# Kernel tuning notes

Measured on AMD Instinct MI355X. Metric: run time of the kernel, lower is better.

## Reference

```python
import jax, jax.numpy as jnp
import numpy as np

B, T, D_IN, H, S, DH = 128, 256, 512, 1024, 128, 1024

def _lin(key, out_d, in_d):
    k = 1.0 / np.sqrt(in_d)
    return jax.random.uniform(key, (out_d, in_d), jnp.float32, -k, k)

def setup_inputs() -> dict:
    key = jax.random.key(0)
    ks = jax.random.split(key, 16)
    kH = 1.0 / np.sqrt(H)
    return {
        'x': jax.random.normal(ks[0], (B, T, D_IN), jnp.float32),
        'noise': jax.random.normal(ks[1], (B, T, S), jnp.float32),
        # LSTM (torch gate order: i, f, g, o)
        'W_ih': _lin(ks[2], 4 * H, S),
        'W_hh': _lin(ks[3], 4 * H, H),
        'b_ih': jax.random.uniform(ks[4], (4 * H,), jnp.float32, -kH, kH),
        'b_hh': jax.random.uniform(ks[5], (4 * H,), jnp.float32, -kH, kH),
        # posterior heads over concat(x_t, h_t): in = H + D_IN
        'Wm': _lin(ks[6], S, H + D_IN), 'bm': jnp.zeros((S,), jnp.float32),
        'Wv': _lin(ks[7], S, H + D_IN), 'bv': jnp.zeros((S,), jnp.float32),
        # decoder MLP
        'Wd1': _lin(ks[8], DH, S), 'bd1': jnp.zeros((DH,), jnp.float32),
        'Wd2': _lin(ks[9], D_IN, DH), 'bd2': jnp.zeros((D_IN,), jnp.float32),
    }

def reference(x, noise, W_ih, W_hh, b_ih, b_hh, Wm, bm, Wv, bv, Wd1, bd1, Wd2, bd2):
    Bb = x.shape[0]
    Hh = W_hh.shape[1]
    Ss = Wm.shape[0]
    dt = x.dtype

    def step(carry, inp):
        h, c, z = carry          # [B,H], [B,H], [B,S]
        xt, nt = inp             # [B,D_IN], [B,S]
        gates = z @ W_ih.T + b_ih + h @ W_hh.T + b_hh   # [B,4H]
        i, f, g, o = jnp.split(gates, 4, axis=-1)
        c = jax.nn.sigmoid(f) * c + jax.nn.sigmoid(i) * jnp.tanh(g)
        h = jax.nn.sigmoid(o) * jnp.tanh(c)
        pi = jnp.concatenate([xt, h], axis=-1)           # [B, D_IN+H]
        mean = pi @ Wm.T + bm
        log_var = pi @ Wv.T + bv
        std = jnp.exp(0.5 * log_var)
        z_new = nt * std + mean
        kl = jnp.sum(std * std + mean * mean - jnp.log(std) - 0.5)
        return (h, c, z_new), (z_new, kl)

    init = (jnp.zeros((Bb, Hh), dt), jnp.zeros((Bb, Hh), dt), jnp.zeros((Bb, Ss), dt))
    xs = (jnp.swapaxes(x, 0, 1), jnp.swapaxes(noise, 0, 1))  # time-major
    _, (zs, kls) = jax.lax.scan(step, init, xs)
    z = jnp.swapaxes(zs, 0, 1)                                # [B,T,S]
    kl = jnp.sum(kls)
    x_hat = jax.nn.relu(z @ Wd1.T + bd1) @ Wd2.T + bd2        # [B,T,D_IN]
    return x_hat, kl
```

## Files before the change

### kernel.cpp

```cpp
#include <hip/hip_runtime.h>
#include <hip/hip_bf16.h>

#define Bdim 128
#define Tdim 256
#define DIN 512
#define Hdim 1024
#define Sdim 128
#define DHdim 1024
#define KG 1152
#define KP 1536
#define NBLK 192
#define LDP 1160

using short8  = __attribute__((ext_vector_type(8))) short;
using floatx4 = __attribute__((ext_vector_type(4))) float;
typedef unsigned long long ull;

#define MFMA(a, b, c) __builtin_amdgcn_mfma_f32_16x16x32_bf16((a), (b), (c), 0, 0, 0)

#define XBF_OFF   0ull
#define WG_OFF    33554432ull
#define WMV_OFF   42991616ull
#define HB_OFF    0ull
#define WD1_OFF   67108864ull
#define WD2_OFF   67371008ull
#define AB_OFF    68419584ull
#define AB_SZ     294912ull
#define ZALL_OFF  69009408ull
#define KL_OFF    77398016ull
#define FLG_OFF   77398144ull

__device__ __forceinline__ float sigf(float v) { return 1.0f / (1.0f + __expf(-v)); }
__device__ __forceinline__ float tanhfast(float v) { return 1.0f - 2.0f / (__expf(2.0f * v) + 1.0f); }

__device__ __forceinline__ short8 cload16(const __hip_bfloat16* p) {
  short8 r;
  asm volatile("global_load_dwordx4 %0, %1, off sc0 sc1" : "=&v"(r) : "v"(p));
  return r;
}
#define VMWAIT0()                                              \
  do {                                                         \
    asm volatile("s_waitcnt vmcnt(0)" ::: "memory");           \
    __builtin_amdgcn_sched_barrier(0);                         \
  } while (0)
#define SB0() __builtin_amdgcn_sched_barrier(0)

__device__ __forceinline__ void astore8(__hip_bfloat16* p, ull v) {
  __hip_atomic_store((ull*)(void*)p, v, __ATOMIC_RELAXED, __HIP_MEMORY_SCOPE_AGENT);
}

__device__ __forceinline__ void waitflags(unsigned* flags, int base, int mask,
                                          unsigned target, int lane) {
  unsigned* p = flags + base + (lane & mask);
  while (!__all((int)(__hip_atomic_load(p, __ATOMIC_RELAXED, __HIP_MEMORY_SCOPE_AGENT) >= target))) {
    __builtin_amdgcn_s_sleep(8);
  }
}

__global__ __launch_bounds__(256) void prep_kernel(
    const float* __restrict__ x, const float* __restrict__ W_ih,
    const float* __restrict__ W_hh, const float* __restrict__ Wm,
    const float* __restrict__ Wv, const float* __restrict__ Wd1,
    const float* __restrict__ Wd2, char* __restrict__ ws) {
  long long i = (long long)blockIdx.x * 256 + threadIdx.x;
  if (i < 16777216LL) {
    ((__hip_bfloat16*)(ws + XBF_OFF))[i] = __float2bfloat16(x[i]);
    return;
  }
  i -= 16777216LL;
  if (i < 4718592LL) {
    int j = (int)(i / KG), k = (int)(i % KG);
    float v = (k < Sdim) ? W_ih[j * Sdim + k] : W_hh[(long long)j * Hdim + (k - Sdim)];
    ((__hip_bfloat16*)(ws + WG_OFF))[i] = __float2bfloat16(v);
    return;
  }
  i -= 4718592LL;
  if (i < 393216LL) {
    int r = (int)(i / KP), k = (int)(i % KP);
    float v = (r < Sdim) ? Wm[r * KP + k] : Wv[(r - Sdim) * KP + k];
    ((__hip_bfloat16*)(ws + WMV_OFF))[i] = __float2bfloat16(v);
    return;
  }
  i -= 393216LL;
  if (i < 131072LL) { ((__hip_bfloat16*)(ws + WD1_OFF))[i] = __float2bfloat16(Wd1[i]); return; }
  i -= 131072LL;
  if (i < 524288LL) { ((__hip_bfloat16*)(ws + WD2_OFF))[i] = __float2bfloat16(Wd2[i]); return; }
  i -= 524288LL;
  if (i < 147456LL) { ((__hip_bfloat16*)(ws + AB_OFF))[i] = __float2bfloat16(0.0f); return; }
  i -= 147456LL;
  if (i == 0) { *((float*)(ws + KL_OFF)) = 0.0f; return; }
  i -= 1;
  if (i < 192LL) { ((unsigned*)(ws + FLG_OFF))[i] = 0u; return; }
}

__global__ __launch_bounds__(256, 1) void scan_kernel(
    char* __restrict__ ws, const float* __restrict__ noise,
    const float* __restrict__ b_ih, const float* __restrict__ b_hh,
    const float* __restrict__ bm, const float* __restrict__ bv) {
  const __hip_bfloat16* WG = (const __hip_bfloat16*)(ws + WG_OFF);
  const __hip_bfloat16* WMV = (const __hip_bfloat16*)(ws + WMV_OFF);
  const __hip_bfloat16* xbf = (const __hip_bfloat16*)(ws + XBF_OFF);
  __hip_bfloat16* zall = (__hip_bfloat16*)(ws + ZALL_OFF);
  float* klacc = (float*)(ws + KL_OFF);
  unsigned* flags = (unsigned*)(ws + FLG_OFF);

  __shared__ __align__(16) char ldsraw[16 * LDP * 2];
  __hip_bfloat16* lds = (__hip_bfloat16*)ldsraw;
  float* smem = (float*)ldsraw;

  const int tid = threadIdx.x;
  const int lane = tid & 63;
  const int w = tid >> 6;
  const int row16 = lane & 15;
  const int quad = lane >> 4;
  const int bid = blockIdx.x;
  const bool is_gates = (bid < 128);

  const __hip_bfloat16* gb_bp[4];
  float biasv[4];
  int mgrp = 0, ns = 0, rowbase = 0;
  float creg[4] = {0.f, 0.f, 0.f, 0.f};
  const __hip_bfloat16* hd_bpm = nullptr;
  const __hip_bfloat16* hd_bpv = nullptr;
  int hd_mb = 0, hd_sb = 0, hd_nx = 0, hd_kbase = 0;
  float hbm = 0.f, hbv = 0.f;
  float klw = 0.f;

  if (is_gates) {
    mgrp = bid >> 4;
    ns = bid & 15;
    rowbase = mgrp * 16;
    #pragma unroll
    for (int j = 0; j < 4; j++) {
      int idx = j * Hdim + ns * 64 + w * 16 + row16;
      gb_bp[j] = WG + (size_t)idx * KG;
      biasv[j] = b_ih[idx] + b_hh[idx];
    }
  } else {
    int hb = bid - 128;
    hd_mb = hb >> 3;
    hd_sb = hb & 7;
    int s = hd_sb * 16 + row16;
    hd_bpm = WMV + (size_t)s * KP;
    hd_bpv = WMV + (size_t)(128 + s) * KP;
    hbm = bm[s];
    hbv = bv[s];
    hd_kbase = w * 384;
    hd_nx = (hd_kbase < DIN) ? ((DIN - hd_kbase) >> 5) : 0;
    if (hd_nx > 12) hd_nx = 12;
  }

  for (int t = 0; t < Tdim; t++) {
    const int par = t & 1;
    const __hip_bfloat16* Ab = (const __hip_bfloat16*)(ws + AB_OFF + (ull)par * AB_SZ);
    __hip_bfloat16* AbW = (__hip_bfloat16*)(ws + AB_OFF + (ull)(par ^ 1) * AB_SZ);

    if (is_gates) {
      floatx4 acc[4];
      #pragma unroll
      for (int j = 0; j < 4; j++)
        acc[j] = (floatx4){biasv[j], biasv[j], biasv[j], biasv[j]};

      if (w == 0) waitflags(flags, mgrp * 16, 15, (unsigned)t, lane);
      __syncthreads();
      {
        short8 sreg[8];
        #pragma unroll
        for (int i = 0; i < 8; i++) {
          int s = tid + i * 256;
          sreg[i] = cload16(Ab + (size_t)(rowbase + (s >> 7)) * KG + Sdim + (s & 127) * 8);
        }
        VMWAIT0();
        #pragma unroll
        for (int i = 0; i < 8; i++) {
          int s = tid + i * 256;
          *(short8*)&lds[(s >> 7) * LDP + Sdim + (s & 127) * 8] = sreg[i];
        }
      }
      __syncthreads();
      #pragma unroll
      for (int c = 0; c < 8; c++) {
        #pragma unroll
        for (int i = 0; i < 4; i++) {
          const int k0 = Sdim + (c * 4 + i) * 32 + quad * 8;
          short8 a = *(const short8*)&lds[row16 * LDP + k0];
          #pragma unroll
          for (int j = 0; j < 4; j++)
            acc[j] = MFMA(a, *(const short8*)(gb_bp[j] + k0), acc[j]);
        }
        SB0();
      }
      if (w == 0) waitflags(flags, 128 + mgrp * 8, 7, (unsigned)t, lane);
      __syncthreads();
      {
        short8 zs = cload16(Ab + (size_t)(rowbase + (tid >> 4)) * KG + (tid & 15) * 8);
        VMWAIT0();
        *(short8*)&lds[(tid >> 4) * LDP + (tid & 15) * 8] = zs;
      }
      __syncthreads();
      #pragma unroll
      for (int kt = 0; kt < 4; kt++) {
        const int k0 = kt * 32 + quad * 8;
        short8 a = *(const short8*)&lds[row16 * LDP + k0];
        #pragma unroll
        for (int j = 0; j < 4; j++)
          acc[j] = MFMA(a, *(const short8*)(gb_bp[j] + k0), acc[j]);
      }
      SB0();
      int hc = ns * 64 + w * 16 + row16;
      #pragma unroll
      for (int r = 0; r < 4; r++) {
        float cn = sigf(acc[1][r]) * creg[r] + sigf(acc[0][r]) * tanhfast(acc[2][r]);
        creg[r] = cn;
        float hn = sigf(acc[3][r]) * tanhfast(cn);
        __hip_bfloat16 hbf = __float2bfloat16(hn);
        unsigned hu = (unsigned)reinterpret_cast<unsigned short&>(hbf);
        unsigned up = hu | (__shfl_xor(hu, 1, 64) << 16);
        unsigned uq = __shfl_xor(up, 2, 64);
        if ((row16 & 3) == 0) {
          int grow = rowbase + quad * 4 + r;
          astore8(AbW + (size_t)grow * KG + Sdim + hc, (ull)up | ((ull)uq << 32));
        }
      }
      __syncthreads();
      if (tid == 0)
        __hip_atomic_store(&flags[bid], (unsigned)(t + 1),
                           __ATOMIC_RELAXED, __HIP_MEMORY_SCOPE_AGENT);
    } else {
      float nz[4];
      if (w == 0) {
        #pragma unroll
        for (int r = 0; r < 4; r++) {
          int b = hd_mb * 16 + quad * 4 + r;
          int s = hd_sb * 16 + row16;
          nz[r] = noise[((size_t)b * Tdim + t) * Sdim + s];
        }
      }
      const __hip_bfloat16* axp = xbf + ((size_t)(hd_mb * 16 + row16) * Tdim + t) * DIN;
      const __hip_bfloat16* ahp = AbW + (size_t)(hd_mb * 16 + row16) * KG + Sdim;
      floatx4 am, av;
      if (w == 0) { am = (floatx4){hbm, hbm, hbm, hbm}; av = (floatx4){hbv, hbv, hbv, hbv}; }
      else        { am = (floatx4){0.f, 0.f, 0.f, 0.f}; av = (floatx4){0.f, 0.f, 0.f, 0.f}; }
      #pragma unroll
      for (int kt = 0; kt < 12; kt++) {
        if (kt < hd_nx) {
          int k0 = hd_kbase + kt * 32 + quad * 8;
          short8 a = *(const short8*)(axp + k0);
          am = MFMA(a, *(const short8*)(hd_bpm + k0), am);
          av = MFMA(a, *(const short8*)(hd_bpv + k0), av);
        }
      }
      if (w == 0) waitflags(flags, hd_mb * 16, 15, (unsigned)(t + 1), lane);
      __syncthreads();
      short8 hreg[12];
      #pragma unroll
      for (int kt = 0; kt < 12; kt++) {
        if (kt >= hd_nx)
          hreg[kt] = cload16(ahp + hd_kbase + kt * 32 + quad * 8 - DIN);
      }
      VMWAIT0();
      #pragma unroll
      for (int kt = 0; kt < 12; kt++) {
        if (kt >= hd_nx) {
          int k0 = hd_kbase + kt * 32 + quad * 8;
          am = MFMA(hreg[kt], *(const short8*)(hd_bpm + k0), am);
          av = MFMA(hreg[kt], *(const short8*)(hd_bpv + k0), av);
        }
      }
      SB0();
      #pragma unroll
      for (int r = 0; r < 4; r++) {
        smem[(w * 2 + 0) * 256 + lane * 4 + r] = am[r];
        smem[(w * 2 + 1) * 256 + lane * 4 + r] = av[r];
      }
      __syncthreads();
      if (w == 0) {
        #pragma unroll
        for (int r = 0; r < 4; r++) {
          int idx = lane * 4 + r;
          float mean = smem[0 * 256 + idx] + smem[2 * 256 + idx] +
                       smem[4 * 256 + idx] + smem[6 * 256 + idx];
          float lv = smem[1 * 256 + idx] + smem[3 * 256 + idx] +
                     smem[5 * 256 + idx] + smem[7 * 256 + idx];
          int b = hd_mb * 16 + quad * 4 + r;
          int s = hd_sb * 16 + row16;
          float std = __expf(0.5f * lv);
          float z = nz[r] * std + mean;
          __hip_bfloat16 zb = __float2bfloat16(z);
          zall[((size_t)b * Tdim + t) * Sdim + s] = zb;
          unsigned zu = (unsigned)reinterpret_cast<unsigned short&>(zb);
          unsigned up = zu | (__shfl_xor(zu, 1, 64) << 16);
          unsigned uq = __shfl_xor(up, 2, 64);
          if ((row16 & 3) == 0)
            astore8(AbW + (size_t)b * KG + s, (ull)up | ((ull)uq << 32));
          klw += std * std + mean * mean - 0.5f * lv - 0.5f;
        }
      }
      __syncthreads();
      if (tid == 0)
        __hip_atomic_store(&flags[bid], (unsigned)(t + 1),
                           __ATOMIC_RELAXED, __HIP_MEMORY_SCOPE_AGENT);
    }
  }
  if (!is_gates && w == 0) {
    #pragma unroll
    for (int off = 32; off > 0; off >>= 1) klw += __shfl_down(klw, off, 64);
    if (lane == 0) atomicAdd(klacc, klw);
  }
}

__global__ __launch_bounds__(256) void dec1_kernel(char* __restrict__ ws,
                                                   const float* __restrict__ bd1) {
  const __hip_bfloat16* zall = (const __hip_bfloat16*)(ws + ZALL_OFF);
  const __hip_bfloat16* Wd1b = (const __hip_bfloat16*)(ws + WD1_OFF);
  __hip_bfloat16* Hbuf = (__hip_bfloat16*)(ws + HB_OFF);
  int tid = threadIdx.x, lane = tid & 63, w = tid >> 6;
  int mb = blockIdx.x, nb = blockIdx.y;
  int row16 = lane & 15, quad = lane >> 4;
  int arow = mb * 64 + w * 16 + row16;
  const __hip_bfloat16* aptr = zall + (size_t)arow * Sdim;
  floatx4 acc[4] = {{0.f,0.f,0.f,0.f},{0.f,0.f,0.f,0.f},{0.f,0.f,0.f,0.f},{0.f,0.f,0.f,0.f}};
  #pragma unroll
  for (int kt = 0; kt < Sdim / 32; kt++) {
    int k0 = kt * 32 + quad * 8;
    short8 a = *(const short8*)(aptr + k0);
    #pragma unroll
    for (int j = 0; j < 4; j++) {
      const __hip_bfloat16* bp = Wd1b + (size_t)(nb * 64 + j * 16 + row16) * Sdim;
      acc[j] = MFMA(a, *(const short8*)(bp + k0), acc[j]);
    }
  }
  #pragma unroll
  for (int j = 0; j < 4; j++) {
    int n = nb * 64 + j * 16 + row16;
    float bias = bd1[n];
    #pragma unroll
    for (int r = 0; r < 4; r++) {
      int rr = mb * 64 + w * 16 + quad * 4 + r;
      float v = fmaxf(acc[j][r] + bias, 0.0f);
      Hbuf[(size_t)rr * DHdim + n] = __float2bfloat16(v);
    }
  }
}

__global__ __launch_bounds__(256) void dec2_kernel(char* __restrict__ ws,
                                                   const float* __restrict__ bd2,
                                                   float* __restrict__ out) {
  const __hip_bfloat16* Hbuf = (const __hip_bfloat16*)(ws + HB_OFF);
  const __hip_bfloat16* Wd2b = (const __hip_bfloat16*)(ws + WD2_OFF);
  int tid = threadIdx.x, lane = tid & 63, w = tid >> 6;
  int mb = blockIdx.x, nb = blockIdx.y;
  int row16 = lane & 15, quad = lane >> 4;
  int arow = mb * 64 + w * 16 + row16;
  const __hip_bfloat16* aptr = Hbuf + (size_t)arow * DHdim;
  const __hip_bfloat16* bp[4];
  #pragma unroll
  for (int j = 0; j < 4; j++) bp[j] = Wd2b + (size_t)(nb * 64 + j * 16 + row16) * DHdim;
  floatx4 acc[4] = {{0.f,0.f,0.f,0.f},{0.f,0.f,0.f,0.f},{0.f,0.f,0.f,0.f},{0.f,0.f,0.f,0.f}};
  for (int kt = 0; kt < DHdim / 32; kt++) {
    int k0 = kt * 32 + quad * 8;
    short8 a = *(const short8*)(aptr + k0);
    #pragma unroll
    for (int j = 0; j < 4; j++)
      acc[j] = MFMA(a, *(const short8*)(bp[j] + k0), acc[j]);
  }
  #pragma unroll
  for (int j = 0; j < 4; j++) {
    int n = nb * 64 + j * 16 + row16;
    float bias = bd2[n];
    #pragma unroll
    for (int r = 0; r < 4; r++) {
      int rr = mb * 64 + w * 16 + quad * 4 + r;
      out[(size_t)rr * DIN + n] = acc[j][r] + bias;
    }
  }
}

__global__ void kl_write_kernel(const char* __restrict__ ws, float* __restrict__ out) {
  if (threadIdx.x == 0 && blockIdx.x == 0)
    out[16777216] = *(const float*)(ws + KL_OFF);
}

extern "C" void kernel_launch(void* const* d_in, const int* in_sizes, int n_in,
                              void* d_out, int out_size, void* d_ws, size_t ws_size,
                              hipStream_t stream) {
  const float* x = (const float*)d_in[0];
  const float* noise = (const float*)d_in[1];
  const float* W_ih = (const float*)d_in[2];
  const float* W_hh = (const float*)d_in[3];
  const float* b_ih = (const float*)d_in[4];
  const float* b_hh = (const float*)d_in[5];
  const float* Wm = (const float*)d_in[6];
  const float* bm = (const float*)d_in[7];
  const float* Wv = (const float*)d_in[8];
  const float* bv = (const float*)d_in[9];
  const float* Wd1 = (const float*)d_in[10];
  const float* bd1 = (const float*)d_in[11];
  const float* Wd2 = (const float*)d_in[12];
  const float* bd2 = (const float*)d_in[13];
  char* ws = (char*)d_ws;
  float* out = (float*)d_out;

  long long total_prep = 22692033LL;
  int pblocks = (int)((total_prep + 255) / 256);
  prep_kernel<<<pblocks, 256, 0, stream>>>(x, W_ih, W_hh, Wm, Wv, Wd1, Wd2, ws);
  scan_kernel<<<NBLK, 256, 0, stream>>>(ws, noise, b_ih, b_hh, bm, bv);
  dec1_kernel<<<dim3(512, 16), 256, 0, stream>>>(ws, bd1);
  dec2_kernel<<<dim3(512, 8), 256, 0, stream>>>(ws, bd2, out);
  kl_write_kernel<<<1, 64, 0, stream>>>(ws, out);
}
```

Before: 5.527 ms.

## Split scan gate K-loop across 8 waves and consolidate head blocks

The persistent scan kernel now runs 512 threads per block. In the gate blocks, two wave halves each take half of the recurrent K dimension, and the partial sums are reduced through LDS before the LSTM cell update. Head blocks drop from 64 to 32; each block handles two S-tiles and stages h into LDS once instead of every wave loading it from global memory. The flag-polling sleep is also shortened. Together these aim to cut per-timestep latency on the serial critical path, at the cost of an extra LDS reduction and more synchronisation per step.

```diff
diff --git a/kernel.cpp b/kernel.cpp
--- a/kernel.cpp
+++ b/kernel.cpp
@@ -9,8 +9,11 @@
 #define DHdim 1024
 #define KG 1152
 #define KP 1536
-#define NBLK 192
+#define GBLK 128
+#define HBLK 32
+#define NBLK 160
 #define LDP 1160
+#define HP  1032
 
 using short8  = __attribute__((ext_vector_type(8))) short;
 using floatx4 = __attribute__((ext_vector_type(4))) float;
@@ -53,7 +56,7 @@
                                           unsigned target, int lane) {
   unsigned* p = flags + base + (lane & mask);
   while (!__all((int)(__hip_atomic_load(p, __ATOMIC_RELAXED, __HIP_MEMORY_SCOPE_AGENT) >= target))) {
-    __builtin_amdgcn_s_sleep(8);
+    __builtin_amdgcn_s_sleep(4);
   }
 }
 
@@ -93,7 +96,7 @@
   if (i < 192LL) { ((unsigned*)(ws + FLG_OFF))[i] = 0u; return; }
 }
 
-__global__ __launch_bounds__(256, 1) void scan_kernel(
+__global__ __launch_bounds__(512, 1) void scan_kernel(
     char* __restrict__ ws, const float* __restrict__ noise,
     const float* __restrict__ b_ih, const float* __restrict__ b_hh,
     const float* __restrict__ bm, const float* __restrict__ bv) {
@@ -104,9 +107,8 @@
   float* klacc = (float*)(ws + KL_OFF);
   unsigned* flags = (unsigned*)(ws + FLG_OFF);
 
-  __shared__ __align__(16) char ldsraw[16 * LDP * 2];
+  __shared__ __align__(16) char ldsraw[57600];
   __hip_bfloat16* lds = (__hip_bfloat16*)ldsraw;
-  float* smem = (float*)ldsraw;
 
   const int tid = threadIdx.x;
   const int lane = tid & 63;
@@ -114,15 +116,15 @@
   const int row16 = lane & 15;
   const int quad = lane >> 4;
   const int bid = blockIdx.x;
-  const bool is_gates = (bid < 128);
+  const bool is_gates = (bid < GBLK);
 
   const __hip_bfloat16* gb_bp[4];
   float biasv[4];
-  int mgrp = 0, ns = 0, rowbase = 0;
+  int mgrp = 0, ns = 0, rowbase = 0, cs = 0, khalf = 0;
   float creg[4] = {0.f, 0.f, 0.f, 0.f};
   const __hip_bfloat16* hd_bpm = nullptr;
   const __hip_bfloat16* hd_bpv = nullptr;
-  int hd_mb = 0, hd_sb = 0, hd_nx = 0, hd_kbase = 0;
+  int hd_mb = 0, hd_pg = 0, hd_nx = 0, hd_kbase = 0, hd_g = 0, hd_stile = 0;
   float hbm = 0.f, hbv = 0.f;
   float klw = 0.f;
 
@@ -130,22 +132,27 @@
     mgrp = bid >> 4;
     ns = bid & 15;
     rowbase = mgrp * 16;
+    cs = w & 3;
+    khalf = w >> 2;
     #pragma unroll
     for (int j = 0; j < 4; j++) {
-      int idx = j * Hdim + ns * 64 + w * 16 + row16;
+      int idx = j * Hdim + ns * 64 + cs * 16 + row16;
       gb_bp[j] = WG + (size_t)idx * KG;
       biasv[j] = b_ih[idx] + b_hh[idx];
     }
   } else {
-    int hb = bid - 128;
-    hd_mb = hb >> 3;
-    hd_sb = hb & 7;
-    int s = hd_sb * 16 + row16;
+    int hb = bid - GBLK;
+    hd_mb = hb >> 2;
+    hd_pg = hb & 3;
+    hd_g = w >> 2;
+    hd_stile = hd_pg * 2 + hd_g;
+    int s = hd_stile * 16 + row16;
     hd_bpm = WMV + (size_t)s * KP;
     hd_bpv = WMV + (size_t)(128 + s) * KP;
     hbm = bm[s];
     hbv = bv[s];
-    hd_kbase = w * 384;
+    int kp = w & 3;
+    hd_kbase = kp * 384;
     hd_nx = (hd_kbase < DIN) ? ((DIN - hd_kbase) >> 5) : 0;
     if (hd_nx > 12) hd_nx = 12;
   }
@@ -156,33 +163,36 @@
     __hip_bfloat16* AbW = (__hip_bfloat16*)(ws + AB_OFF + (ull)(par ^ 1) * AB_SZ);
 
     if (is_gates) {
+      float* rsm = (float*)(ldsraw + 37120);
       floatx4 acc[4];
       #pragma unroll
       for (int j = 0; j < 4; j++)
-        acc[j] = (floatx4){biasv[j], biasv[j], biasv[j], biasv[j]};
+        acc[j] = (khalf == 0)
+          ? (floatx4){biasv[j], biasv[j], biasv[j], biasv[j]}
+          : (floatx4){0.f, 0.f, 0.f, 0.f};
 
       if (w == 0) waitflags(flags, mgrp * 16, 15, (unsigned)t, lane);
       __syncthreads();
       {
-        short8 sreg[8];
-        #pragma unroll
-        for (int i = 0; i < 8; i++) {
-          int s = tid + i * 256;
+        short8 sreg[4];
+        #pragma unroll
+        for (int i = 0; i < 4; i++) {
+          int s = tid + i * 512;
           sreg[i] = cload16(Ab + (size_t)(rowbase + (s >> 7)) * KG + Sdim + (s & 127) * 8);
         }
         VMWAIT0();
         #pragma unroll
-        for (int i = 0; i < 8; i++) {
-          int s = tid + i * 256;
+        for (int i = 0; i < 4; i++) {
+          int s = tid + i * 512;
           *(short8*)&lds[(s >> 7) * LDP + Sdim + (s & 127) * 8] = sreg[i];
         }
       }
       __syncthreads();
       #pragma unroll
-      for (int c = 0; c < 8; c++) {
+      for (int c = 0; c < 4; c++) {
         #pragma unroll
         for (int i = 0; i < 4; i++) {
-          const int k0 = Sdim + (c * 4 + i) * 32 + quad * 8;
+          const int k0 = Sdim + (khalf * 16 + c * 4 + i) * 32 + quad * 8;
           short8 a = *(const short8*)&lds[row16 * LDP + k0];
           #pragma unroll
           for (int j = 0; j < 4; j++)
@@ -190,36 +200,45 @@
         }
         SB0();
       }
-      if (w == 0) waitflags(flags, 128 + mgrp * 8, 7, (unsigned)t, lane);
-      __syncthreads();
-      {
-        short8 zs = cload16(Ab + (size_t)(rowbase + (tid >> 4)) * KG + (tid & 15) * 8);
+      if (khalf == 1) {
+        #pragma unroll
+        for (int j = 0; j < 4; j++)
+          *(floatx4*)&rsm[cs * 1280 + lane * 20 + j * 4] = acc[j];
+      }
+      if (w == 0) waitflags(flags, GBLK + mgrp * 4, 3, (unsigned)t, lane);
+      __syncthreads();
+      if (khalf == 0) {
+        const __hip_bfloat16* zp = Ab + (size_t)(rowbase + row16) * KG;
+        short8 zreg[4];
+        #pragma unroll
+        for (int kt = 0; kt < 4; kt++)
+          zreg[kt] = cload16(zp + kt * 32 + quad * 8);
         VMWAIT0();
-        *(short8*)&lds[(tid >> 4) * LDP + (tid & 15) * 8] = zs;
-      }
-      __syncthreads();
-      #pragma unroll
-      for (int kt = 0; kt < 4; kt++) {
-        const int k0 = kt * 32 + quad * 8;
-        short8 a = *(const short8*)&lds[row16 * LDP + k0];
+        #pragma unroll
+        for (int kt = 0; kt < 4; kt++) {
+          const int k0 = kt * 32 + quad * 8;
+          #pragma unroll
+          for (int j = 0; j < 4; j++)
+            acc[j] = MFMA(zreg[kt], *(const short8*)(gb_bp[j] + k0), acc[j]);
+        }
+        SB0();
         #pragma unroll
         for (int j = 0; j < 4; j++)
-          acc[j] = MFMA(a, *(const short8*)(gb_bp[j] + k0), acc[j]);
-      }
-      SB0();
-      int hc = ns * 64 + w * 16 + row16;
-      #pragma unroll
-      for (int r = 0; r < 4; r++) {
-        float cn = sigf(acc[1][r]) * creg[r] + sigf(acc[0][r]) * tanhfast(acc[2][r]);
-        creg[r] = cn;
-        float hn = sigf(acc[3][r]) * tanhfast(cn);
-        __hip_bfloat16 hbf = __float2bfloat16(hn);
-        unsigned hu = (unsigned)reinterpret_cast<unsigned short&>(hbf);
-        unsigned up = hu | (__shfl_xor(hu, 1, 64) << 16);
-        unsigned uq = __shfl_xor(up, 2, 64);
-        if ((row16 & 3) == 0) {
-          int grow = rowbase + quad * 4 + r;
-          astore8(AbW + (size_t)grow * KG + Sdim + hc, (ull)up | ((ull)uq << 32));
+          acc[j] += *(const floatx4*)&rsm[cs * 1280 + lane * 20 + j * 4];
+        #pragma unroll
+        for (int r = 0; r < 4; r++) {
+          float cn = sigf(acc[1][r]) * creg[r] + sigf(acc[0][r]) * tanhfast(acc[2][r]);
+          creg[r] = cn;
+          float hn = sigf(acc[3][r]) * tanhfast(cn);
+          __hip_bfloat16 hbf = __float2bfloat16(hn);
+          unsigned hu = (unsigned)reinterpret_cast<unsigned short&>(hbf);
+          unsigned up = hu | (__shfl_xor(hu, 1, 64) << 16);
+          unsigned uq = __shfl_xor(up, 2, 64);
+          if ((row16 & 3) == 0) {
+            int grow = rowbase + quad * 4 + r;
+            int hc = ns * 64 + cs * 16 + row16;
+            astore8(AbW + (size_t)grow * KG + Sdim + hc, (ull)up | ((ull)uq << 32));
+          }
         }
       }
       __syncthreads();
@@ -227,63 +246,79 @@
         __hip_atomic_store(&flags[bid], (unsigned)(t + 1),
                            __ATOMIC_RELAXED, __HIP_MEMORY_SCOPE_AGENT);
     } else {
+      float* smf = (float*)(ldsraw + 33024);
       float nz[4];
-      if (w == 0) {
+      if ((w & 3) == 0) {
         #pragma unroll
         for (int r = 0; r < 4; r++) {
           int b = hd_mb * 16 + quad * 4 + r;
-          int s = hd_sb * 16 + row16;
+          int s = hd_stile * 16 + row16;
           nz[r] = noise[((size_t)b * Tdim + t) * Sdim + s];
         }
       }
       const __hip_bfloat16* axp = xbf + ((size_t)(hd_mb * 16 + row16) * Tdim + t) * DIN;
-      const __hip_bfloat16* ahp = AbW + (size_t)(hd_mb * 16 + row16) * KG + Sdim;
-      floatx4 am, av;
-      if (w == 0) { am = (floatx4){hbm, hbm, hbm, hbm}; av = (floatx4){hbv, hbv, hbv, hbv}; }
-      else        { am = (floatx4){0.f, 0.f, 0.f, 0.f}; av = (floatx4){0.f, 0.f, 0.f, 0.f}; }
-      #pragma unroll
-      for (int kt = 0; kt < 12; kt++) {
-        if (kt < hd_nx) {
-          int k0 = hd_kbase + kt * 32 + quad * 8;
-          short8 a = *(const short8*)(axp + k0);
-          am = MFMA(a, *(const short8*)(hd_bpm + k0), am);
-          av = MFMA(a, *(const short8*)(hd_bpv + k0), av);
+      floatx4 am = {0.f, 0.f, 0.f, 0.f}, av = {0.f, 0.f, 0.f, 0.f};
+      {
+        short8 areg[12];
+        #pragma unroll
+        for (int kt = 0; kt < 12; kt++)
+          if (kt < hd_nx)
+            areg[kt] = *(const short8*)(axp + hd_kbase + kt * 32 + quad * 8);
+        #pragma unroll
+        for (int kt = 0; kt < 12; kt++) {
+          if (kt < hd_nx) {
+            int k0 = hd_kbase + kt * 32 + quad * 8;
+            am = MFMA(areg[kt], *(const short8*)(hd_bpm + k0), am);
+            av = MFMA(areg[kt], *(const short8*)(hd_bpv + k0), av);
+          }
         }
       }
       if (w == 0) waitflags(flags, hd_mb * 16, 15, (unsigned)(t + 1), lane);
       __syncthreads();
-      short8 hreg[12];
-      #pragma unroll
-      for (int kt = 0; kt < 12; kt++) {
-        if (kt >= hd_nx)
-          hreg[kt] = cload16(ahp + hd_kbase + kt * 32 + quad * 8 - DIN);
-      }
-      VMWAIT0();
+      {
+        short8 sreg[4];
+        #pragma unroll
+        for (int i = 0; i < 4; i++) {
+          int s = tid + i * 512;
+          sreg[i] = cload16(AbW + (size_t)(hd_mb * 16 + (s >> 7)) * KG + Sdim + (s & 127) * 8);
+        }
+        VMWAIT0();
+        #pragma unroll
+        for (int i = 0; i < 4; i++) {
+          int s = tid + i * 512;
+          *(short8*)&lds[(s >> 7) * HP + (s & 127) * 8] = sreg[i];
+        }
+      }
+      __syncthreads();
       #pragma unroll
       for (int kt = 0; kt < 12; kt++) {
         if (kt >= hd_nx) {
           int k0 = hd_kbase + kt * 32 + quad * 8;
-          am = MFMA(hreg[kt], *(const short8*)(hd_bpm + k0), am);
-          av = MFMA(hreg[kt], *(const short8*)(hd_bpv + k0), av);
+          short8 a = *(const short8*)&lds[row16 * HP + (k0 - DIN)];
+          am = MFMA(a, *(const short8*)(hd_bpm + k0), am);
+          av = MFMA(a, *(const short8*)(hd_bpv + k0), av);
         }
       }
       SB0();
-      #pragma unroll
-      for (int r = 0; r < 4; r++) {
-        smem[(w * 2 + 0) * 256 + lane * 4 + r] = am[r];
-        smem[(w * 2 + 1) * 256 + lane * 4 + r] = av[r];
-      }
-      __syncthreads();
-      if (w == 0) {
+      {
+        int kp = w & 3;
+        #pragma unroll
+        for (int r = 0; r < 4; r++) {
+          smf[hd_g * 2048 + (kp * 2 + 0) * 256 + lane * 4 + r] = am[r];
+          smf[hd_g * 2048 + (kp * 2 + 1) * 256 + lane * 4 + r] = av[r];
+        }
+      }
+      __syncthreads();
+      if ((w & 3) == 0) {
         #pragma unroll
         for (int r = 0; r < 4; r++) {
           int idx = lane * 4 + r;
-          float mean = smem[0 * 256 + idx] + smem[2 * 256 + idx] +
-                       smem[4 * 256 + idx] + smem[6 * 256 + idx];
-          float lv = smem[1 * 256 + idx] + smem[3 * 256 + idx] +
-                     smem[5 * 256 + idx] + smem[7 * 256 + idx];
+          float mean = hbm + smf[hd_g * 2048 + 0 * 256 + idx] + smf[hd_g * 2048 + 2 * 256 + idx] +
+                       smf[hd_g * 2048 + 4 * 256 + idx] + smf[hd_g * 2048 + 6 * 256 + idx];
+          float lv = hbv + smf[hd_g * 2048 + 1 * 256 + idx] + smf[hd_g * 2048 + 3 * 256 + idx] +
+                     smf[hd_g * 2048 + 5 * 256 + idx] + smf[hd_g * 2048 + 7 * 256 + idx];
           int b = hd_mb * 16 + quad * 4 + r;
-          int s = hd_sb * 16 + row16;
+          int s = hd_stile * 16 + row16;
           float std = __expf(0.5f * lv);
           float z = nz[r] * std + mean;
           __hip_bfloat16 zb = __float2bfloat16(z);
@@ -302,7 +337,7 @@
                            __ATOMIC_RELAXED, __HIP_MEMORY_SCOPE_AGENT);
     }
   }
-  if (!is_gates && w == 0) {
+  if (!is_gates && (w & 3) == 0) {
     #pragma unroll
     for (int off = 32; off > 0; off >>= 1) klw += __shfl_down(klw, off, 64);
     if (lane == 0) atomicAdd(klacc, klw);
@@ -404,7 +439,7 @@
   long long total_prep = 22692033LL;
   int pblocks = (int)((total_prep + 255) / 256);
   prep_kernel<<<pblocks, 256, 0, stream>>>(x, W_ih, W_hh, Wm, Wv, Wd1, Wd2, ws);
-  scan_kernel<<<NBLK, 256, 0, stream>>>(ws, noise, b_ih, b_hh, bm, bv);
+  scan_kernel<<<NBLK, 512, 0, stream>>>(ws, noise, b_ih, b_hh, bm, bv);
   dec1_kernel<<<dim3(512, 16), 256, 0, stream>>>(ws, bd1);
   dec2_kernel<<<dim3(512, 8), 256, 0, stream>>>(ws, bd2, out);
   kl_write_kernel<<<1, 64, 0, stream>>>(ws, out);
```

New measurement: 5.630 ms. Within noise of the previous version (+1.9%).
